# Kernel optimization log

Measured on AMD Instinct MI355X. Metric: run time of the kernel, lower is better.

The kernel has to match this reference:

```python
import jax, jax.numpy as jnp
import numpy as np

N, E = 50000, 800000
IN, HID, OUT = 128, 256, 128
BN_EPS = 1e-5


def setup_inputs() -> dict:
    key = jax.random.key(0)
    ks = jax.random.split(key, 12)
    x = jax.random.normal(ks[0], (N, IN), dtype=jnp.float32)
    edge_index = jax.random.randint(ks[1], (2, E), 0, N, dtype=jnp.int64)
    edge_weight = jax.random.uniform(ks[2], (E,), dtype=jnp.float32)
    # GCNConv weights (glorot-ish scale) and biases
    W0 = jax.random.normal(ks[3], (IN, HID), dtype=jnp.float32) * (1.0 / np.sqrt(IN))
    b0 = jnp.zeros((HID,), jnp.float32)
    W1 = jax.random.normal(ks[4], (HID, HID), dtype=jnp.float32) * (1.0 / np.sqrt(HID))
    b1 = jnp.zeros((HID,), jnp.float32)
    Wl = jax.random.normal(ks[5], (HID, OUT), dtype=jnp.float32) * (1.0 / np.sqrt(HID))
    bl = jnp.zeros((OUT,), jnp.float32)
    # BatchNorm affine params (eval mode: running_mean=0, running_var=1)
    g0 = 1.0 + 0.1 * jax.random.normal(ks[6], (HID,), dtype=jnp.float32)
    be0 = 0.1 * jax.random.normal(ks[7], (HID,), dtype=jnp.float32)
    g1 = 1.0 + 0.1 * jax.random.normal(ks[8], (HID,), dtype=jnp.float32)
    be1 = 0.1 * jax.random.normal(ks[9], (HID,), dtype=jnp.float32)
    return {"x": x, "edge_index": edge_index, "edge_weight": edge_weight,
            "W0": W0, "b0": b0, "W1": W1, "b1": b1, "Wl": Wl, "bl": bl,
            "g0": g0, "be0": be0, "g1": g1, "be1": be1}


def reference(x, edge_index, edge_weight, W0, b0, W1, b1, Wl, bl, g0, be0, g1, be1):
    n = x.shape[0]
    row, col = edge_index[0], edge_index[1]
    # add self-loops with weight 1 (GCNConv default)
    ar = jnp.arange(n)
    rowf = jnp.concatenate([row, ar])
    colf = jnp.concatenate([col, ar])
    wf = jnp.concatenate([edge_weight, jnp.ones((n,), x.dtype)])
    # symmetric normalization: D^{-1/2} A D^{-1/2}
    deg = jax.ops.segment_sum(wf, colf, num_segments=n)
    dinv = jnp.where(deg > 0, jax.lax.rsqrt(deg), 0.0)
    norm = dinv[rowf] * wf * dinv[colf]  # [E+N]

    def conv(h, W, b):
        h = h @ W                       # [n, d_out]
        msg = h[rowf] * norm[:, None]   # gather + scale per edge
        return jax.ops.segment_sum(msg, colf, num_segments=n) + b

    def bn_eval(h, g, b):
        # eval-mode BN with running_mean=0, running_var=1
        return h * (g / jnp.sqrt(1.0 + BN_EPS)) + b

    h = jax.nn.relu(bn_eval(conv(x, W0, b0), g0, be0))
    h = jax.nn.relu(bn_eval(conv(h, W1, b1), g1, be1))
    h = conv(h, Wl, bl)
    return jax.nn.log_softmax(h, axis=1)
```

## Files before the change

kernel.cpp:

```cpp
#include <hip/hip_runtime.h>
#include <cstddef>
#include <cstdint>


#define GCN_BN_EPS 1e-5f
#define NB_CHUNK 256

typedef short v8bf __attribute__((ext_vector_type(8)));
typedef float v4f __attribute__((ext_vector_type(4)));


__device__ __forceinline__ float4 unpack_bf4(uint2 u) {
  float4 r;
  r.x = __uint_as_float(u.x << 16);
  r.y = __uint_as_float(u.x & 0xffff0000u);
  r.z = __uint_as_float(u.y << 16);
  r.w = __uint_as_float(u.y & 0xffff0000u);
  return r;
}
__device__ __forceinline__ uint16_t f2bf(float f) {
  uint32_t u = __float_as_uint(f);
  return (uint16_t)((u + 0x7fffu + ((u >> 16) & 1u)) >> 16);
}
__device__ __forceinline__ uint2 pack_bf4(float4 v) {
  uint2 r;
  r.x = (uint32_t)f2bf(v.x) | ((uint32_t)f2bf(v.y) << 16);
  r.y = (uint32_t)f2bf(v.z) | ((uint32_t)f2bf(v.w) << 16);
  return r;
}


__global__ __launch_bounds__(256) void build_hist_kernel(
    const int* __restrict__ ei, const float* __restrict__ ew,
    int* __restrict__ col_, uint2* __restrict__ pk,
    unsigned int* __restrict__ histw, int E, int n) {
  extern __shared__ unsigned int h8[];
  __shared__ int s_flag;
  const int b = blockIdx.x;
  const int nw = (n + 3) >> 2;
  if (threadIdx.x == 0) {
    int nz = 0;
    for (int k = 1; k < 64; k += 2) nz |= ei[k];
    s_flag = (nz == 0) ? 1 : 0;
  }
  for (int i = threadIdx.x; i < nw; i += 256) h8[i] = 0u;
  __syncthreads();
  const int flag = s_flag;
  const int per = (E + NB_CHUNK - 1) / NB_CHUNK;
  const int e0 = b * per, e1 = min(e0 + per, E);
  for (int e = e0 + threadIdx.x; e < e1; e += 256) {
    int r, c;
    if (flag) { r = ei[2 * e]; c = ei[2 * (E + e)]; }
    else      { r = ei[e];     c = ei[E + e]; }
    col_[e] = c;
    pk[e] = make_uint2((unsigned)r, __float_as_uint(ew[e]));
    atomicAdd(&h8[c >> 2], 1u << ((c & 3) * 8));
  }
  __syncthreads();
  for (int i = threadIdx.x; i < nw; i += 256)
    histw[(size_t)b * nw + i] = h8[i];
}

__global__ __launch_bounds__(256) void scan1_conv_kernel(
    const unsigned int* __restrict__ histw, unsigned int* __restrict__ cntw,
    int* __restrict__ bsum, int nw, int nB,
    const float* __restrict__ x, uint16_t* __restrict__ xb,
    const float* __restrict__ W0, uint16_t* __restrict__ W0t,
    const float* __restrict__ W1, uint16_t* __restrict__ W1t,
    const float* __restrict__ Wl, uint16_t* __restrict__ Wlt,
    int t0, int convTot) {
  if (blockIdx.x >= nB) {
    int i = (blockIdx.x - nB) * 256 + threadIdx.x;
    if (i >= convTot) return;
    if (i < t0) {
      float4 v = *(const float4*)&x[(size_t)i * 4];
      *(uint2*)&xb[(size_t)i * 4] = pack_bf4(v);
      return;
    }
    int j = i - t0;
    if (j < 128 * 256) { int nn = j >> 7, k = j & 127; W0t[j] = f2bf(W0[(size_t)k * 256 + nn]); return; }
    j -= 128 * 256;
    if (j < 256 * 256) { int nn = j >> 8, k = j & 255; W1t[j] = f2bf(W1[(size_t)k * 256 + nn]); return; }
    j -= 256 * 256;
    if (j < 256 * 128) { int nn = j >> 8, k = j & 255; Wlt[j] = f2bf(Wl[(size_t)k * 128 + nn]); }
    return;
  }
  __shared__ int ws[4];
  const int j = blockIdx.x * 256 + threadIdx.x;
  unsigned int acc = 0;
  if (j < nw)
    for (int b = 0; b < NB_CHUNK; ++b) acc += histw[(size_t)b * nw + j];
  if (j < nw) cntw[j] = acc;
  int s = (int)((acc & 0xffu) + ((acc >> 8) & 0xffu) + ((acc >> 16) & 0xffu) + (acc >> 24));
  int x_ = s;
#pragma unroll
  for (int st = 1; st < 64; st <<= 1) x_ += __shfl_xor(x_, st, 64);
  if ((threadIdx.x & 63) == 0) ws[threadIdx.x >> 6] = x_;
  __syncthreads();
  if (threadIdx.x == 0) bsum[blockIdx.x] = ws[0] + ws[1] + ws[2] + ws[3];
}

__global__ __launch_bounds__(256) void scan3_base_kernel(
    const unsigned int* __restrict__ cntw, const int* __restrict__ bsum,
    int* __restrict__ off, unsigned int* __restrict__ histw,
    int nw, int nB, int n, int E) {
  __shared__ int wsum[4], woff[4];
  __shared__ int s_gbase;
  const int tid = threadIdx.x, lane = tid & 63, wv = tid >> 6;
  const int j = blockIdx.x * 256 + tid;
  unsigned int cw = (j < nw) ? cntw[j] : 0u;
  const int c0 = (int)(cw & 0xffu), c1 = (int)((cw >> 8) & 0xffu);
  const int c2 = (int)((cw >> 16) & 0xffu), c3 = (int)(cw >> 24);
  int s = c0 + c1 + c2 + c3;
  int x = s;
#pragma unroll
  for (int st = 1; st < 64; st <<= 1) { int t = __shfl_up(x, st, 64); if (lane >= st) x += t; }
  if (lane == 63) wsum[wv] = x;
  __syncthreads();
  if (tid == 0) { int r = 0; for (int k = 0; k < 4; ++k) { woff[k] = r; r += wsum[k]; } }
  if (wv == 0) {
    int v2 = (lane < nB) ? bsum[lane] : 0;
    int y = v2;
#pragma unroll
    for (int st = 1; st < 64; st <<= 1) { int t = __shfl_up(y, st, 64); if (lane >= st) y += t; }
    if (lane == blockIdx.x) s_gbase = y - v2;
  }
  __syncthreads();
  if (j < nw) {
    int excl = x - s + woff[wv] + s_gbase;
    uint4 o4;
    o4.x = excl; o4.y = excl + c0; o4.z = excl + c0 + c1; o4.w = excl + c0 + c1 + c2;
    *(uint4*)&off[4 * j] = o4;
    unsigned int run = 0;
    for (int b = 0; b < NB_CHUNK; ++b) {
      size_t idx = (size_t)b * nw + j;
      unsigned int w = histw[idx];
      histw[idx] = run;
      run += w;
    }
  }
  if (blockIdx.x == 0 && tid == 0) off[n] = E;
}

__global__ __launch_bounds__(256) void fill_kernel(
    const int* __restrict__ col_, const uint2* __restrict__ pk,
    const int* __restrict__ off, const unsigned int* __restrict__ histw,
    uint2* __restrict__ csr, int E, int n) {
  extern __shared__ unsigned int c8[];
  const int b = blockIdx.x;
  const int nw = (n + 3) >> 2;
  for (int i = threadIdx.x; i < nw; i += 256) c8[i] = 0u;
  __syncthreads();
  const int per = (E + NB_CHUNK - 1) / NB_CHUNK;
  const int e0 = b * per, e1 = min(e0 + per, E);
  const unsigned int* brel = histw + (size_t)b * nw;
  for (int e = e0 + threadIdx.x; e < e1; e += 256) {
    int c = col_[e];
    const int sh = (c & 3) * 8;
    unsigned old = atomicAdd(&c8[c >> 2], 1u << sh);
    int rel = (int)((old >> sh) & 0xffu) + (int)((brel[c >> 2] >> sh) & 0xffu);
    csr[off[c] + rel] = pk[e];
  }
}

__global__ void degdinv_kernel(const int* __restrict__ off, const uint2* __restrict__ csr,
                               float* __restrict__ dinv, int n) {
  int i = blockIdx.x * blockDim.x + threadIdx.x;
  if (i >= n) return;
  float s = 1.0f;
  int p1 = off[i + 1];
  for (int p = off[i]; p < p1; ++p) s += __uint_as_float(csr[p].y);
  dinv[i] = rsqrtf(s);
}

__global__ void val_kernel(const int* __restrict__ off, uint2* __restrict__ csr,
                           const float* __restrict__ dinv, int n) {
  int i = blockIdx.x * blockDim.x + threadIdx.x;
  if (i >= n) return;
  float dc = dinv[i];
  int p1 = off[i + 1];
  for (int p = off[i]; p < p1; ++p) {
    uint2 t = csr[p];
    csr[p].y = __float_as_uint(dinv[t.x] * __uint_as_float(t.y) * dc);
  }
}


template <int EPI>
__global__ __launch_bounds__(256) void agg256_kernel(
    const uint16_t* __restrict__ hin, uint16_t* __restrict__ hout,
    const int* __restrict__ off, const uint2* __restrict__ csr,
    const float* __restrict__ dinv,
    const float* __restrict__ bias, const float* __restrict__ g,
    const float* __restrict__ be, int n) {
  const int lane = threadIdx.x & 63;
  const int c = blockIdx.x * 4 + (threadIdx.x >> 6);
  if (c >= n) return;
  const int f = lane * 4;
  const int e0 = off[c], e1 = off[c + 1];
  const float di = dinv[c];
  const float s2 = di * di;
  float4 self = unpack_bf4(*(const uint2*)&hin[(size_t)c * 256 + f]);
  float4 acc = make_float4(self.x * s2, self.y * s2, self.z * s2, self.w * s2);

  for (int base = e0; base < e1; base += 64) {
    int idx = base + lane;
    int rs = 0; float rv = 0.0f;
    if (idx < e1) { uint2 ev = csr[idx]; rs = (int)ev.x; rv = __uint_as_float(ev.y); }
    const int m = min(64, e1 - base);
    const int nG = (m + 3) >> 2;
    for (int gI = 0; gI < nG; ++gI) {
      int e_ = gI * 4;
      int s0 = __shfl(rs, e_);     float v0 = __shfl(rv, e_);
      int s1 = __shfl(rs, e_ + 1); float v1 = __shfl(rv, e_ + 1);
      int sB = __shfl(rs, e_ + 2); float v2 = __shfl(rv, e_ + 2);
      int s3 = __shfl(rs, e_ + 3); float v3 = __shfl(rv, e_ + 3);
      float4 h0 = unpack_bf4(*(const uint2*)&hin[(size_t)s0 * 256 + f]);
      float4 h1 = unpack_bf4(*(const uint2*)&hin[(size_t)s1 * 256 + f]);
      float4 h2 = unpack_bf4(*(const uint2*)&hin[(size_t)sB * 256 + f]);
      float4 h3 = unpack_bf4(*(const uint2*)&hin[(size_t)s3 * 256 + f]);
      acc.x += v0 * h0.x + v1 * h1.x + v2 * h2.x + v3 * h3.x;
      acc.y += v0 * h0.y + v1 * h1.y + v2 * h2.y + v3 * h3.y;
      acc.z += v0 * h0.z + v1 * h1.z + v2 * h2.z + v3 * h3.z;
      acc.w += v0 * h0.w + v1 * h1.w + v2 * h2.w + v3 * h3.w;
    }
  }

  if (EPI == 1) {
    const float bns = rsqrtf(1.0f + GCN_BN_EPS);
    float4 bi = *(const float4*)&bias[f];
    float4 gi = *(const float4*)&g[f];
    float4 bei = *(const float4*)&be[f];
    acc.x = fmaxf((acc.x + bi.x) * gi.x * bns + bei.x, 0.0f);
    acc.y = fmaxf((acc.y + bi.y) * gi.y * bns + bei.y, 0.0f);
    acc.z = fmaxf((acc.z + bi.z) * gi.z * bns + bei.z, 0.0f);
    acc.w = fmaxf((acc.w + bi.w) * gi.w * bns + bei.w, 0.0f);
  }
  *(uint2*)&hout[(size_t)c * 256 + f] = pack_bf4(acc);
}

template <int EPI>
__global__ __launch_bounds__(256) void agg128_kernel(
    const uint16_t* __restrict__ hin, void* __restrict__ hout_,
    const int* __restrict__ off, const uint2* __restrict__ csr,
    const float* __restrict__ dinv,
    const float* __restrict__ bias, int n) {
  const int lane = threadIdx.x & 63;
  const int sub = lane & 31;
  const int hbase = lane & 32;
  const int c = blockIdx.x * 8 + (threadIdx.x >> 6) * 2 + (lane >> 5);
  const bool active = (c < n);
  const int f = sub * 4;

  int e0 = 0, e1 = 0;
  float4 acc = make_float4(0.f, 0.f, 0.f, 0.f);
  if (active) {
    e0 = off[c]; e1 = off[c + 1];
    float di = dinv[c];
    float s2 = di * di;
    float4 self = unpack_bf4(*(const uint2*)&hin[(size_t)c * 128 + f]);
    acc = make_float4(self.x * s2, self.y * s2, self.z * s2, self.w * s2);
  }
  int nch = (e1 - e0 + 31) >> 5;
  nch = max(nch, __shfl(nch, lane ^ 32));

  for (int ch = 0; ch < nch; ++ch) {
    int idx = e0 + ch * 32 + sub;
    int rs = 0; float rv = 0.0f;
    if (active && idx < e1) { uint2 ev = csr[idx]; rs = (int)ev.x; rv = __uint_as_float(ev.y); }
    int m = e1 - (e0 + ch * 32);
    m = m < 0 ? 0 : (m > 32 ? 32 : m);
    int mMax = max(m, __shfl(m, lane ^ 32));
    const int nG = (mMax + 3) >> 2;
    for (int gI = 0; gI < nG; ++gI) {
      int e_ = hbase + gI * 4;
      int s0 = __shfl(rs, e_);     float v0 = __shfl(rv, e_);
      int s1 = __shfl(rs, e_ + 1); float v1 = __shfl(rv, e_ + 1);
      int sB = __shfl(rs, e_ + 2); float v2 = __shfl(rv, e_ + 2);
      int s3 = __shfl(rs, e_ + 3); float v3 = __shfl(rv, e_ + 3);
      float4 h0 = unpack_bf4(*(const uint2*)&hin[(size_t)s0 * 128 + f]);
      float4 h1 = unpack_bf4(*(const uint2*)&hin[(size_t)s1 * 128 + f]);
      float4 h2 = unpack_bf4(*(const uint2*)&hin[(size_t)sB * 128 + f]);
      float4 h3 = unpack_bf4(*(const uint2*)&hin[(size_t)s3 * 128 + f]);
      acc.x += v0 * h0.x + v1 * h1.x + v2 * h2.x + v3 * h3.x;
      acc.y += v0 * h0.y + v1 * h1.y + v2 * h2.y + v3 * h3.y;
      acc.z += v0 * h0.z + v1 * h1.z + v2 * h2.z + v3 * h3.z;
      acc.w += v0 * h0.w + v1 * h1.w + v2 * h2.w + v3 * h3.w;
    }
  }

  if (EPI == 0) {
    uint16_t* hout = (uint16_t*)hout_;
    if (active) *(uint2*)&hout[(size_t)c * 128 + f] = pack_bf4(acc);
  } else {
    float* hout = (float*)hout_;
    float4 bi = active ? *(const float4*)&bias[f] : make_float4(0.f, 0.f, 0.f, 0.f);
    float tx = acc.x + bi.x, ty = acc.y + bi.y, tz = acc.z + bi.z, tw = acc.w + bi.w;
    float mx = fmaxf(fmaxf(tx, ty), fmaxf(tz, tw));
#pragma unroll
    for (int s = 1; s < 32; s <<= 1) mx = fmaxf(mx, __shfl_xor(mx, s, 64));
    float ex = expf(tx - mx) + expf(ty - mx) + expf(tz - mx) + expf(tw - mx);
#pragma unroll
    for (int s = 1; s < 32; s <<= 1) ex += __shfl_xor(ex, s, 64);
    float lse = logf(ex) + mx;
    if (active) {
      float4 res = make_float4(tx - lse, ty - lse, tz - lse, tw - lse);
      *(float4*)&hout[(size_t)c * 128 + f] = res;
    }
  }
}

template <int K, int NC, int EPI>
__global__ __launch_bounds__(256) void mfma_gemm_kernel(
    const uint16_t* __restrict__ A, const uint16_t* __restrict__ WT,
    uint16_t* __restrict__ Cb, int M, int tpb,
    const float* __restrict__ bias, const float* __restrict__ g,
    const float* __restrict__ be) {
  constexpr int CW = NC / 4;
  constexpr int NT = CW / 16;
  constexpr int KS = K / 32;
  const int lane = threadIdx.x & 63;
  const int wave = threadIdx.x >> 6;
  const int quad = lane >> 4;
  const int l16 = lane & 15;
  const int col0 = wave * CW;

  const int tiles = (M + 15) >> 4;
  int t0 = blockIdx.x * tpb;
  if (t0 >= tiles) return;
  int t1 = min(t0 + tpb, tiles);

  v8bf b[KS][NT];
#pragma unroll
  for (int ks = 0; ks < KS; ++ks)
#pragma unroll
    for (int nt = 0; nt < NT; ++nt)
      b[ks][nt] = *(const v8bf*)(WT + (size_t)(col0 + nt * 16 + l16) * K +
                                 ks * 32 + quad * 8);

  float sc[NT], o1[NT], o2[NT];
  if (EPI == 1) {
    const float bns = rsqrtf(1.0f + GCN_BN_EPS);
#pragma unroll
    for (int nt = 0; nt < NT; ++nt) {
      int col = col0 + nt * 16 + l16;
      sc[nt] = g[col] * bns; o1[nt] = bias[col]; o2[nt] = be[col];
    }
  }

  v8bf a[KS], an[KS];
  {
    int arow = min(t0 * 16 + l16, M - 1);
    const uint16_t* Ap = A + (size_t)arow * K + quad * 8;
#pragma unroll
    for (int ks = 0; ks < KS; ++ks) a[ks] = *(const v8bf*)(Ap + ks * 32);
  }
  for (int t = t0; t < t1; ++t) {
    if (t + 1 < t1) {
      int arow = min((t + 1) * 16 + l16, M - 1);
      const uint16_t* Ap = A + (size_t)arow * K + quad * 8;
#pragma unroll
      for (int ks = 0; ks < KS; ++ks) an[ks] = *(const v8bf*)(Ap + ks * 32);
    }
    v4f acc[NT];
#pragma unroll
    for (int nt = 0; nt < NT; ++nt) acc[nt] = (v4f){0.f, 0.f, 0.f, 0.f};
#pragma unroll
    for (int ks = 0; ks < KS; ++ks)
#pragma unroll
      for (int nt = 0; nt < NT; ++nt)
        acc[nt] = __builtin_amdgcn_mfma_f32_16x16x32_bf16(a[ks], b[ks][nt],
                                                          acc[nt], 0, 0, 0);
    const int row0 = t * 16 + quad * 4;
#pragma unroll
    for (int nt = 0; nt < NT; ++nt) {
      const int col = col0 + nt * 16 + l16;
#pragma unroll
      for (int r = 0; r < 4; ++r) {
        int row = row0 + r;
        if (row < M) {
          float v = acc[nt][r];
          if (EPI == 1) v = fmaxf((v + o1[nt]) * sc[nt] + o2[nt], 0.0f);
          Cb[(size_t)row * NC + col] = f2bf(v);
        }
      }
    }
#pragma unroll
    for (int ks = 0; ks < KS; ++ks) a[ks] = an[ks];
  }
}


static inline char* carve(char*& p, size_t bytes) {
  char* r = p;
  p += (bytes + 255) & ~(size_t)255;
  return r;
}

extern "C" void kernel_launch(void* const* d_in, const int* in_sizes, int n_in,
                              void* d_out, int out_size, void* d_ws, size_t ws_size,
                              hipStream_t stream) {
  const int N = in_sizes[0] / 128;
  const int E = in_sizes[2];

  const float* x  = (const float*)d_in[0];
  const int*   ei = (const int*)d_in[1];
  const float* ew = (const float*)d_in[2];
  const float* W0 = (const float*)d_in[3];
  const float* b0 = (const float*)d_in[4];
  const float* W1 = (const float*)d_in[5];
  const float* b1 = (const float*)d_in[6];
  const float* Wl = (const float*)d_in[7];
  const float* bl = (const float*)d_in[8];
  const float* g0 = (const float*)d_in[9];
  const float* be0 = (const float*)d_in[10];
  const float* g1 = (const float*)d_in[11];
  const float* be1 = (const float*)d_in[12];
  float* out = (float*)d_out;

  const int nw = (N + 3) / 4;

  char* p = (char*)d_ws;
  float*        dinv  = (float*)carve(p, (size_t)N * 4);
  unsigned int* cntw  = (unsigned int*)carve(p, (size_t)nw * 4);
  int*          off   = (int*)carve(p, (size_t)(N + 1) * 4);
  int*          bsum  = (int*)carve(p, 1024 * 4);
  int*          col_  = (int*)carve(p, (size_t)E * 4);
  uint2*        pk    = (uint2*)carve(p, (size_t)E * 8);
  uint2*        csr   = (uint2*)carve(p, (size_t)E * 8);
  unsigned int* histw = (unsigned int*)carve(p, (size_t)NB_CHUNK * nw * 4);
  uint16_t*     xb16  = (uint16_t*)carve(p, (size_t)N * 128 * 2);
  uint16_t*     bufR  = (uint16_t*)carve(p, (size_t)N * 128 * 2);
  uint16_t*     bufP  = (uint16_t*)carve(p, (size_t)N * 256 * 2);
  uint16_t*     bufQ  = (uint16_t*)carve(p, (size_t)N * 256 * 2);
  uint16_t*     W0t   = (uint16_t*)carve(p, (size_t)128 * 256 * 2);
  uint16_t*     W1t   = (uint16_t*)carve(p, (size_t)256 * 256 * 2);
  uint16_t*     Wlt   = (uint16_t*)carve(p, (size_t)256 * 128 * 2);

  const int TB = 256;
  const int gN = (N + TB - 1) / TB;
  const int gW4 = (N + 3) / 4;
  const int gW8 = (N + 7) / 8;
  const int tiles = (N + 15) / 16;
  const int TPB = 8;
  const int gG = (tiles + TPB - 1) / TPB;
  const size_t ldsU8 = (size_t)nw * 4;
  const int nB = (nw + 255) / 256;
  const int convT0 = N * 32;
  const int convTot = convT0 + 128 * 256 + 256 * 256 + 256 * 128;
  const int convB = (convTot + TB - 1) / TB;

  build_hist_kernel<<<NB_CHUNK, TB, ldsU8, stream>>>(ei, ew, col_, pk, histw, E, N);
  scan1_conv_kernel<<<nB + convB, TB, 0, stream>>>(histw, cntw, bsum, nw, nB,
                                                   x, xb16, W0, W0t, W1, W1t,
                                                   Wl, Wlt, convT0, convTot);
  scan3_base_kernel<<<nB, TB, 0, stream>>>(cntw, bsum, off, histw, nw, nB, N, E);
  fill_kernel<<<NB_CHUNK, TB, ldsU8, stream>>>(col_, pk, off, histw, csr, E, N);
  degdinv_kernel<<<gN, TB, 0, stream>>>(off, csr, dinv, N);
  val_kernel<<<gN, TB, 0, stream>>>(off, csr, dinv, N);

  agg128_kernel<0><<<gW8, 256, 0, stream>>>(xb16, bufR, off, csr, dinv, nullptr, N);
  mfma_gemm_kernel<128, 256, 1><<<gG, 256, 0, stream>>>(bufR, W0t, bufP, N, TPB,
                                                        b0, g0, be0);
  mfma_gemm_kernel<256, 256, 0><<<gG, 256, 0, stream>>>(bufP, W1t, bufQ, N, TPB,
                                                        nullptr, nullptr, nullptr);
  agg256_kernel<1><<<gW4, 256, 0, stream>>>(bufQ, bufP, off, csr, dinv,
                                            b1, g1, be1, N);
  mfma_gemm_kernel<256, 128, 0><<<gG, 256, 0, stream>>>(bufP, Wlt, bufR, N, TPB,
                                                        nullptr, nullptr, nullptr);
  agg128_kernel<2><<<gW8, 256, 0, stream>>>(bufR, out, off, csr, dinv, bl, N);
}
```

Baseline: 361.2 us.

## Factor symmetric normalization into row pre/post scaling and drop edge-value pass

Splits the D^-1/2 A D^-1/2 normalization into two row scalings. Source features are pre-scaled by dinv: for x inside the fused degree kernel, and for later layers in the GEMM epilogue. Aggregated outputs are then post-scaled by dinv[c]. This removes the val_kernel pass that rewrote every CSR value with a gathered dinv[src], and folds the x-to-bf16 conversion into the degree kernel. The cost is one extra per-row multiply in the GEMM and aggregation epilogues, plus slightly different bf16 rounding because scaled values are stored in bf16.

Result: slower. 388.1 us (+7.4%).

```diff
diff --git a/kernel.cpp b/kernel.cpp
--- a/kernel.cpp
+++ b/kernel.cpp
@@ -64,20 +64,13 @@
 __global__ __launch_bounds__(256) void scan1_conv_kernel(
     const unsigned int* __restrict__ histw, unsigned int* __restrict__ cntw,
     int* __restrict__ bsum, int nw, int nB,
-    const float* __restrict__ x, uint16_t* __restrict__ xb,
     const float* __restrict__ W0, uint16_t* __restrict__ W0t,
     const float* __restrict__ W1, uint16_t* __restrict__ W1t,
     const float* __restrict__ Wl, uint16_t* __restrict__ Wlt,
-    int t0, int convTot) {
+    int convTot) {
   if (blockIdx.x >= nB) {
-    int i = (blockIdx.x - nB) * 256 + threadIdx.x;
-    if (i >= convTot) return;
-    if (i < t0) {
-      float4 v = *(const float4*)&x[(size_t)i * 4];
-      *(uint2*)&xb[(size_t)i * 4] = pack_bf4(v);
-      return;
-    }
-    int j = i - t0;
+    int j = (blockIdx.x - nB) * 256 + threadIdx.x;
+    if (j >= convTot) return;
     if (j < 128 * 256) { int nn = j >> 7, k = j & 127; W0t[j] = f2bf(W0[(size_t)k * 256 + nn]); return; }
     j -= 128 * 256;
     if (j < 256 * 256) { int nn = j >> 8, k = j & 255; W1t[j] = f2bf(W1[(size_t)k * 256 + nn]); return; }
@@ -163,25 +156,32 @@
   }
 }
 
-__global__ void degdinv_kernel(const int* __restrict__ off, const uint2* __restrict__ csr,
-                               float* __restrict__ dinv, int n) {
-  int i = blockIdx.x * blockDim.x + threadIdx.x;
-  if (i >= n) return;
-  float s = 1.0f;
-  int p1 = off[i + 1];
-  for (int p = off[i]; p < p1; ++p) s += __uint_as_float(csr[p].y);
-  dinv[i] = rsqrtf(s);
-}
-
-__global__ void val_kernel(const int* __restrict__ off, uint2* __restrict__ csr,
-                           const float* __restrict__ dinv, int n) {
-  int i = blockIdx.x * blockDim.x + threadIdx.x;
-  if (i >= n) return;
-  float dc = dinv[i];
-  int p1 = off[i + 1];
-  for (int p = off[i]; p < p1; ++p) {
-    uint2 t = csr[p];
-    csr[p].y = __float_as_uint(dinv[t.x] * __uint_as_float(t.y) * dc);
+__global__ __launch_bounds__(256) void degdinv_convx_kernel(
+    const int* __restrict__ off, const uint2* __restrict__ csr,
+    float* __restrict__ dinv, const float* __restrict__ x,
+    uint16_t* __restrict__ xb, int n) {
+  __shared__ float sdi[256];
+  const int base = blockIdx.x * 256;
+  const int i = base + threadIdx.x;
+  float di = 0.0f;
+  if (i < n) {
+    float s = 1.0f;
+    int p1 = off[i + 1];
+    for (int p = off[i]; p < p1; ++p) s += __uint_as_float(csr[p].y);
+    di = rsqrtf(s);
+    dinv[i] = di;
+  }
+  sdi[threadIdx.x] = di;
+  __syncthreads();
+  const int nn = min(256, n - base);
+  const int tot = nn * 32;
+  for (int j = threadIdx.x; j < tot; j += 256) {
+    int node = j >> 5, grp = j & 31;
+    float dv = sdi[node];
+    size_t idx = ((size_t)(base + node) * 32 + grp) * 4;
+    float4 v = *(const float4*)&x[idx];
+    v.x *= dv; v.y *= dv; v.z *= dv; v.w *= dv;
+    *(uint2*)&xb[idx] = pack_bf4(v);
   }
 }
 
@@ -199,9 +199,7 @@
   const int f = lane * 4;
   const int e0 = off[c], e1 = off[c + 1];
   const float di = dinv[c];
-  const float s2 = di * di;
-  float4 self = unpack_bf4(*(const uint2*)&hin[(size_t)c * 256 + f]);
-  float4 acc = make_float4(self.x * s2, self.y * s2, self.z * s2, self.w * s2);
+  float4 acc = unpack_bf4(*(const uint2*)&hin[(size_t)c * 256 + f]);
 
   for (int base = e0; base < e1; base += 64) {
     int idx = base + lane;
@@ -226,6 +224,7 @@
     }
   }
 
+  acc.x *= di; acc.y *= di; acc.z *= di; acc.w *= di;
   if (EPI == 1) {
     const float bns = rsqrtf(1.0f + GCN_BN_EPS);
     float4 bi = *(const float4*)&bias[f];
@@ -253,13 +252,12 @@
   const int f = sub * 4;
 
   int e0 = 0, e1 = 0;
+  float di = 0.0f;
   float4 acc = make_float4(0.f, 0.f, 0.f, 0.f);
   if (active) {
     e0 = off[c]; e1 = off[c + 1];
-    float di = dinv[c];
-    float s2 = di * di;
-    float4 self = unpack_bf4(*(const uint2*)&hin[(size_t)c * 128 + f]);
-    acc = make_float4(self.x * s2, self.y * s2, self.z * s2, self.w * s2);
+    di = dinv[c];
+    acc = unpack_bf4(*(const uint2*)&hin[(size_t)c * 128 + f]);
   }
   int nch = (e1 - e0 + 31) >> 5;
   nch = max(nch, __shfl(nch, lane ^ 32));
@@ -289,6 +287,7 @@
     }
   }
 
+  acc.x *= di; acc.y *= di; acc.z *= di; acc.w *= di;
   if (EPI == 0) {
     uint16_t* hout = (uint16_t*)hout_;
     if (active) *(uint2*)&hout[(size_t)c * 128 + f] = pack_bf4(acc);
@@ -315,7 +314,7 @@
     const uint16_t* __restrict__ A, const uint16_t* __restrict__ WT,
     uint16_t* __restrict__ Cb, int M, int tpb,
     const float* __restrict__ bias, const float* __restrict__ g,
-    const float* __restrict__ be) {
+    const float* __restrict__ be, const float* __restrict__ dinv) {
   constexpr int CW = NC / 4;
   constexpr int NT = CW / 16;
   constexpr int KS = K / 32;
@@ -372,6 +371,12 @@
         acc[nt] = __builtin_amdgcn_mfma_f32_16x16x32_bf16(a[ks], b[ks][nt],
                                                           acc[nt], 0, 0, 0);
     const int row0 = t * 16 + quad * 4;
+    float dv[4];
+    if (EPI == 2) {
+#pragma unroll
+      for (int r = 0; r < 4; ++r)
+        dv[r] = (row0 + r < M) ? dinv[row0 + r] : 0.0f;
+    }
 #pragma unroll
     for (int nt = 0; nt < NT; ++nt) {
       const int col = col0 + nt * 16 + l16;
@@ -381,6 +386,7 @@
         if (row < M) {
           float v = acc[nt][r];
           if (EPI == 1) v = fmaxf((v + o1[nt]) * sc[nt] + o2[nt], 0.0f);
+          if (EPI == 2) v *= dv[r];
           Cb[(size_t)row * NC + col] = f2bf(v);
         }
       }
@@ -446,27 +452,27 @@
   const int gG = (tiles + TPB - 1) / TPB;
   const size_t ldsU8 = (size_t)nw * 4;
   const int nB = (nw + 255) / 256;
-  const int convT0 = N * 32;
-  const int convTot = convT0 + 128 * 256 + 256 * 256 + 256 * 128;
+  const int convTot = 128 * 256 + 256 * 256 + 256 * 128;
   const int convB = (convTot + TB - 1) / TB;
 
   build_hist_kernel<<<NB_CHUNK, TB, ldsU8, stream>>>(ei, ew, col_, pk, histw, E, N);
   scan1_conv_kernel<<<nB + convB, TB, 0, stream>>>(histw, cntw, bsum, nw, nB,
-                                                   x, xb16, W0, W0t, W1, W1t,
-                                                   Wl, Wlt, convT0, convTot);
+                                                   W0, W0t, W1, W1t, Wl, Wlt,
+                                                   convTot);
   scan3_base_kernel<<<nB, TB, 0, stream>>>(cntw, bsum, off, histw, nw, nB, N, E);
   fill_kernel<<<NB_CHUNK, TB, ldsU8, stream>>>(col_, pk, off, histw, csr, E, N);
-  degdinv_kernel<<<gN, TB, 0, stream>>>(off, csr, dinv, N);
-  val_kernel<<<gN, TB, 0, stream>>>(off, csr, dinv, N);
+  degdinv_convx_kernel<<<gN, TB, 0, stream>>>(off, csr, dinv, x, xb16, N);
 
   agg128_kernel<0><<<gW8, 256, 0, stream>>>(xb16, bufR, off, csr, dinv, nullptr, N);
   mfma_gemm_kernel<128, 256, 1><<<gG, 256, 0, stream>>>(bufR, W0t, bufP, N, TPB,
-                                                        b0, g0, be0);
-  mfma_gemm_kernel<256, 256, 0><<<gG, 256, 0, stream>>>(bufP, W1t, bufQ, N, TPB,
-                                                        nullptr, nullptr, nullptr);
+                                                        b0, g0, be0, nullptr);
+  mfma_gemm_kernel<256, 256, 2><<<gG, 256, 0, stream>>>(bufP, W1t, bufQ, N, TPB,
+                                                        nullptr, nullptr, nullptr,
+                                                        dinv);
   agg256_kernel<1><<<gW4, 256, 0, stream>>>(bufQ, bufP, off, csr, dinv,
                                             b1, g1, be1, N);
-  mfma_gemm_kernel<256, 128, 0><<<gG, 256, 0, stream>>>(bufP, Wlt, bufR, N, TPB,
-                                                        nullptr, nullptr, nullptr);
+  mfma_gemm_kernel<256, 128, 2><<<gG, 256, 0, stream>>>(bufP, Wlt, bufR, N, TPB,
+                                                        nullptr, nullptr, nullptr,
+                                                        dinv);
   agg128_kernel<2><<<gW8, 256, 0, stream>>>(bufR, out, off, csr, dinv, bl, N);
 }
```
